# Kernel optimization log

Hardware: AMD Instinct MI355X
Metric: run time of the kernel (lower is better)

## Reference

```python
import jax, jax.numpy as jnp
import numpy as np

TAG_THR = 0.1
MIN_HEIGHT = 0.0
PULL_WEIGHT = 1.0
PUSH_WEIGHT = 1.0
EPS = 1e-6


def _bbox_iou(boxes):
    # boxes: [N,4] -> IoU [N,N] (standard, no +1 offset; heights in the loss
    # are also computed without +1)
    x1, y1, x2, y2 = boxes[:, 0], boxes[:, 1], boxes[:, 2], boxes[:, 3]
    area = (x2 - x1) * (y2 - y1)
    iw = jnp.clip(jnp.minimum(x2[:, None], x2[None, :]) - jnp.maximum(x1[:, None], x1[None, :]), 0.0)
    ih = jnp.clip(jnp.minimum(y2[:, None], y2[None, :]) - jnp.maximum(y1[:, None], y1[None, :]), 0.0)
    inter = iw * ih
    union = area[:, None] + area[None, :] - inter
    return inter / jnp.maximum(union, 1e-12)


def _single_image(pred, gt_inds, proposals):
    # pred [N,D], gt_inds [N] int, proposals [N,5]
    N = pred.shape[0]
    heights = proposals[:, 3] - proposals[:, 1]
    valid = (gt_inds >= 0) & (heights > MIN_HEIGHT)
    scores = proposals[:, 4]
    iou = _bbox_iou(proposals[:, :4])  # [N,N]

    def step(state, _):
        alive, tot_pull, tot_push, pull_cnt, push_cnt = state
        active = jnp.sum(alive) >= 2  # pop i; if nothing remains, the torch loop breaks
        # i = highest-scoring remaining proposal (greedy, score-sorted)
        i = jnp.argmax(jnp.where(alive, scores, -jnp.inf))
        rem = alive.at[i].set(False)
        overlap = (iou[i] > 0.0) & rem
        diff = jnp.mean((pred - pred[i]) ** 2, axis=1)  # [N]
        check = diff < TAG_THR
        same = gt_inds == gt_inds[i]
        pull_m = overlap & same & ~check
        push_m = overlap & ~same & check
        pn = jnp.sum(pull_m)
        qn = jnp.sum(push_m)
        pull_l = jnp.sum(jnp.where(pull_m, diff * scores, 0.0)) / jnp.maximum(pn, 1).astype(diff.dtype)
        push_l = jnp.sum(jnp.where(push_m, jnp.exp(-diff) * scores, 0.0)) / jnp.maximum(qn, 1).astype(diff.dtype)
        add_pull = active & (pn > 0)
        add_push = active & (qn > 0)
        tot_pull = tot_pull + jnp.where(add_pull, pull_l, 0.0)
        tot_push = tot_push + jnp.where(add_push, push_l, 0.0)
        pull_cnt = pull_cnt + add_pull.astype(jnp.float32)
        push_cnt = push_cnt + add_push.astype(jnp.float32)
        # suppress everything overlapping i whose tag is already close (diff < thr)
        new_alive = rem & ~(overlap & check)
        alive = jnp.where(active, new_alive, alive)
        return (alive, tot_pull, tot_push, pull_cnt, push_cnt), None

    z = jnp.float32(0.0)
    init = (valid, z, z, z, z)
    (_, tot_pull, tot_push, pull_cnt, push_cnt), _ = jax.lax.scan(step, init, None, length=N)
    pull = tot_pull / (pull_cnt + EPS)
    push = tot_push / (push_cnt + EPS)
    return push, pull


def setup_inputs() -> dict:
    key = jax.random.key(0)
    k1, k2, k3, k4, k5, k6, k7 = jax.random.split(key, 7)
    IMGS, N, D = 4, 2000, 4
    pred = jax.random.normal(k1, (IMGS, N, D), dtype=jnp.float32)
    gt_inds = jax.random.randint(k2, (IMGS, N), 0, 50, dtype=jnp.int32)
    x1 = jax.random.uniform(k3, (IMGS, N), minval=0.0, maxval=800.0)
    y1 = jax.random.uniform(k4, (IMGS, N), minval=0.0, maxval=800.0)
    w = jax.random.uniform(k5, (IMGS, N), minval=8.0, maxval=128.0)
    h = jax.random.uniform(k6, (IMGS, N), minval=8.0, maxval=128.0)
    score = jax.random.uniform(k7, (IMGS, N), minval=0.0, maxval=1.0)
    proposals = jnp.stack([x1, y1, x1 + w, y1 + h, score], axis=-1).astype(jnp.float32)
    gt_bboxes = jax.random.uniform(jax.random.fold_in(key, 9), (IMGS, 20, 4), dtype=jnp.float32)
    return {"pred": pred, "gt_inds": gt_inds, "proposals": proposals, "gt_bboxes": gt_bboxes}


def reference(pred, gt_inds, proposals, gt_bboxes):
    # gt_bboxes is accepted by the torch forward but never used in the loss math.
    push, pull = jax.vmap(_single_image)(pred, gt_inds, proposals)  # per-image scalars
    img_num = pred.shape[0]
    push_loss = jnp.sum(push) / img_num * PUSH_WEIGHT
    pull_loss = jnp.sum(pull) / img_num * PULL_WEIGHT
    return push_loss, pull_loss
```

## Files before the change

### kernel.cpp

```cpp
#include <hip/hip_runtime.h>
#include <stdint.h>

#define BLOCK 256
#define KMAX 8
#define NWAVES (BLOCK / 64)
#define S2 2048
#define NW 32
#define NCH 32
#define SPB 16
#define PB (S2 / SPB)
#define RB (S2 / BLOCK)
#define PCAP 65536
#define LDSP2 4096
#define BCAP 64
#define EFF_INF 0x7FFFFFFF

__global__ __launch_bounds__(BLOCK) void rankcount_kernel(
    const float* __restrict__ proposals,
    int* __restrict__ partial, int* __restrict__ pcnt,
    float* __restrict__ acc, int* __restrict__ done, int N, int imgs)
{
    const int bi = blockIdx.x, bj = blockIdx.y, img = blockIdx.z;
    const int t = threadIdx.x;
    if (bi == 0 && bj == 0 && img == 0) {
        if (t < imgs) pcnt[t] = 0;
        if (t >= 64 && t < 64 + imgs*4) acc[t - 64] = 0.f;
        if (t == 128) *done = 0;
    }
    const float* P = proposals + (size_t)img * N * 5;
    __shared__ unsigned sj[BLOCK];
    const int jbase = bj * BLOCK;
    {
        int j = jbase + t;
        sj[t] = (j < N) ? __float_as_uint(P[j*5 + 4]) : 0u;
    }
    __syncthreads();
    const int i = bi * BLOCK + t;
    if (i >= N) return;
    const unsigned my = __float_as_uint(P[i*5 + 4]);
    int p = 0;
    const uint4* s4 = (const uint4*)sj;
#pragma unroll
    for (int q = 0; q < BLOCK/4; ++q) {
        uint4 v = s4[q];
        int jj = jbase + q*4;
        p += (int)((v.x > my) | ((v.x == my) & (jj + 0 < i)));
        p += (int)((v.y > my) | ((v.y == my) & (jj + 1 < i)));
        p += (int)((v.z > my) | ((v.z == my) & (jj + 2 < i)));
        p += (int)((v.w > my) | ((v.w == my) & (jj + 3 < i)));
    }
    partial[((size_t)(img*RB + bj))*S2 + i] = p;
}

__global__ __launch_bounds__(BLOCK) void rankscatter_kernel(
    const float* __restrict__ pred, const int* __restrict__ gt_inds,
    const float* __restrict__ proposals, const int* __restrict__ partial,
    float* __restrict__ soa, int* __restrict__ sgt, int N, int imgs)
{
    const int img = blockIdx.y, t = threadIdx.x;
    const int i = blockIdx.x * BLOCK + t;
    const size_t stride = (size_t)imgs * S2;
    const size_t base   = (size_t)img * S2;

    if (i >= N) {
        if (i < S2) {
#pragma unroll
            for (int a = 0; a < 9; ++a) soa[(size_t)a*stride + base + i] = 0.f;
            sgt[base + i] = -1;
        }
        return;
    }

    const float* P = proposals + (size_t)img * N * 5;
    const float* E = pred      + (size_t)img * N * 4;
    const int*   G = gt_inds   + (size_t)img * N;

    const float p0 = P[i*5+0], p1 = P[i*5+1], p2 = P[i*5+2],
                p3 = P[i*5+3], p4 = P[i*5+4];
    const float q0 = E[i*4+0], q1 = E[i*4+1], q2 = E[i*4+2], q3 = E[i*4+3];
    const int   gg = G[i];

    int p = 0;
#pragma unroll
    for (int b = 0; b < RB; ++b)
        p += partial[((size_t)(img*RB + b))*S2 + i];

    soa[0*stride + base + p] = p0;
    soa[1*stride + base + p] = p1;
    soa[2*stride + base + p] = p2;
    soa[3*stride + base + p] = p3;
    soa[4*stride + base + p] = p4;
    soa[5*stride + base + p] = q0;
    soa[6*stride + base + p] = q1;
    soa[7*stride + base + p] = q2;
    soa[8*stride + base + p] = q3;
    sgt[base + p] = gg;
}

__global__ __launch_bounds__(BLOCK) void suppairs_kernel(
    const float* __restrict__ soa, unsigned* __restrict__ pairs,
    int* __restrict__ pcnt, int N, int imgs)
{
    const int ic = blockIdx.x, jc = blockIdx.y, img = blockIdx.z;
    if (ic < jc) return;
    const int t = threadIdx.x, wave = t >> 6, lane = t & 63;
    const size_t stride = (size_t)imgs * S2, base = (size_t)img * S2;
    __shared__ float si[8][64];
    for (int idx = t; idx < 512; idx += BLOCK) {
        int f = idx >> 6, e = idx & 63;
        int a = (f < 4) ? f : f + 1;
        si[f][e] = soa[(size_t)a*stride + base + ic*64 + e];
    }
    __syncthreads();
    const int j = jc*64 + lane;
    const float jx1 = soa[0*stride+base+j], jy1 = soa[1*stride+base+j];
    const float jx2 = soa[2*stride+base+j], jy2 = soa[3*stride+base+j];
    const float j0  = soa[5*stride+base+j], j1  = soa[6*stride+base+j];
    const float j2  = soa[7*stride+base+j], j3  = soa[8*stride+base+j];
    const bool jin = (j < N);
    unsigned* PL = pairs + (size_t)img * PCAP;
    for (int ii = 0; ii < 16; ++ii) {
        int il = wave*16 + ii;
        int i  = ic*64 + il;
        bool s = false;
        if (jin && i < N && i > j) {
            float iw = fminf(jx2, si[2][il]) - fmaxf(jx1, si[0][il]);
            float ih = fminf(jy2, si[3][il]) - fmaxf(jy1, si[1][il]);
            if (iw > 0.f && ih > 0.f) {
                float d0 = j0-si[4][il], d1 = j1-si[5][il];
                float d2 = j2-si[6][il], d3 = j3-si[7][il];
                float diff = 0.25f*(d0*d0 + d1*d1 + d2*d2 + d3*d3);
                s = diff < 0.1f;
            }
        }
        unsigned long long m = __ballot(s);
        if (m) {
            int leader = __ffsll((unsigned long long)m) - 1;
            int basei = 0;
            if (lane == leader) basei = atomicAdd(&pcnt[img], __popcll(m));
            basei = __shfl(basei, leader);
            if (s) {
                int idx = basei + __popcll(m & ((lane == 0) ? 0ull : (~0ull >> (64 - lane))));
                if (idx < PCAP) PL[idx] = ((unsigned)j << 11) | (unsigned)i;
            }
        }
    }
}

__global__ __launch_bounds__(BLOCK) void greedyeff_kernel(
    const unsigned* __restrict__ pairs, const int* __restrict__ pcnt,
    const int* __restrict__ sgt, const float* __restrict__ soa,
    unsigned long long* __restrict__ selw, int* __restrict__ eff,
    int* __restrict__ nsteps, int imgs)
{
    const int img = blockIdx.x, t = threadIdx.x;
    const int lane = t & 63, wave = t >> 6;
    const size_t stride = (size_t)imgs * S2, base = (size_t)img * S2;

    __shared__ __align__(16) char A[16384];
    __shared__ unsigned spair[LDSP2];
    __shared__ unsigned bucket[NCH * BCAP];
    __shared__ int bcnt[NCH];
    __shared__ unsigned long long skilled[NW], ssel[NW], svalid[NW];
    __shared__ int pfx[NW + 1];
    __shared__ unsigned wsum[NWAVES];
    __shared__ int bm[NWAVES];
    __shared__ int sV;

    unsigned long long* slocAll = (unsigned long long*)A;

    int P = pcnt[img]; if (P > PCAP) P = PCAP;
    const unsigned* PL = pairs + (size_t)img * PCAP;
    const bool staged = (P <= LDSP2);

    for (int x = t; x < S2; x += BLOCK) slocAll[x] = 0ull;
    if (t < NCH) bcnt[t] = 0;
    if (t == 0) sV = 0;
    __syncthreads();
    if (staged) for (int p = t; p < P; p += BLOCK) spair[p] = PL[p];
    for (int g = wave; g < NCH; g += NWAVES) {
        int j = g*64 + lane;
        int gv = sgt[base + j];
        float a = soa[1*stride + base + j];
        float b = soa[3*stride + base + j];
        bool invalid = !(gv >= 0 && (b - a) > 0.f);
        unsigned long long bb = __ballot(invalid);
        if (lane == 0) {
            skilled[g] = bb;
            svalid[g] = ~bb;
            atomicAdd(&sV, 64 - __popcll(bb));
        }
    }
    __syncthreads();
    for (int p = t; p < P; p += BLOCK) {
        unsigned v = staged ? spair[p] : PL[p];
        int lo = v >> 11, hi = v & 2047;
        if ((lo >> 6) == (hi >> 6)) {
            atomicOr(&slocAll[hi], 1ull << (lo & 63));
        } else {
            int idx = atomicAdd(&bcnt[lo >> 6], 1);
            if (idx < BCAP) bucket[(lo >> 6)*BCAP + idx] = v;
        }
    }
    __syncthreads();

    if (wave == 0) {
        const unsigned long long lowmask = (lane == 0) ? 0ull : (~0ull >> (64 - lane));
        for (int c = 0; c < NCH; ++c) {
            unsigned long long U = ~skilled[c];
            const unsigned long long loc = slocAll[c*64 + lane];
            unsigned long long sel = 0ull;
            while (U) {
                bool inU = (U >> lane) & 1ull;
                unsigned long long Am = __ballot(inU && ((loc & U & lowmask) == 0ull));
                sel |= Am;
                bool kill = inU && !((Am >> lane) & 1ull) && ((loc & Am) != 0ull);
                unsigned long long K = __ballot(kill);
                U &= ~(Am | K);
            }
            if (lane == 0) ssel[c] = sel;
            if (sel != 0ull) {
                const int bc = bcnt[c];
                if (bc <= BCAP) {
                    for (int q = lane; q < bc; q += 64) {
                        unsigned v = bucket[c*BCAP + q];
                        int lo = v >> 11, hi = v & 2047;
                        if ((sel >> (lo & 63)) & 1ull)
                            atomicOr(&skilled[hi >> 6], 1ull << (hi & 63));
                    }
                } else {
                    for (int p = lane; p < P; p += 64) {
                        unsigned v = PL[p];
                        int lo = v >> 11, hi = v & 2047;
                        if ((lo >> 6) == c && (hi >> 6) != c &&
                            ((sel >> (lo & 63)) & 1ull))
                            atomicOr(&skilled[hi >> 6], 1ull << (hi & 63));
                    }
                }
            }
        }
    }
    __syncthreads();
    if (t < NW) selw[(size_t)img*NW + t] = ssel[t];

    int* sistar = (int*)A;
    unsigned* hist = (unsigned*)(A + 8192);
    for (int x = t; x < S2; x += BLOCK) { sistar[x] = EFF_INF; hist[x] = 0u; }
    if (t == 0) {
        int s = 0;
        for (int w = 0; w < NW; ++w) { pfx[w] = s; s += __popcll(ssel[w]); }
        pfx[NW] = s;
    }
    __syncthreads();
    for (int p = t; p < P; p += BLOCK) {
        unsigned v = staged ? spair[p] : PL[p];
        int lo = v >> 11, hi = v & 2047;
        if ((ssel[lo >> 6] >> (lo & 63)) & 1ull) atomicMin(&sistar[hi], lo);
    }
    __syncthreads();
#pragma unroll
    for (int k = 0; k < 8; ++k) {
        const int j = k*BLOCK + t;
        const int jw = j >> 6, jb = j & 63;
        bool valid = (svalid[jw] >> jb) & 1ull;
        bool selb  = (ssel[jw] >> jb) & 1ull;
        int e;
        if (!valid) e = 0;
        else if (selb)
            e = pfx[jw] + __popcll(ssel[jw] & (jb ? (~0ull >> (64 - jb)) : 0ull));
        else {
            int is = sistar[j];
            if (is == EFF_INF) e = EFF_INF;
            else {
                int iw_ = is >> 6, ib = is & 63;
                e = pfx[iw_] + __popcll(ssel[iw_] & (ib ? (~0ull >> (64 - ib)) : 0ull)) + 1;
                atomicAdd(&hist[e - 1], 1u);
            }
        }
        eff[(size_t)img*S2 + j] = e;
    }
    __syncthreads();

    const int V = sV, Sc = pfx[NW];
    unsigned loc8[8]; unsigned s = 0;
#pragma unroll
    for (int k = 0; k < 8; ++k) { s += hist[t*8 + k]; loc8[k] = s; }
    unsigned tot = s;
    for (int o = 1; o < 64; o <<= 1) {
        unsigned u = __shfl_up(tot, o);
        if (lane >= o) tot += u;
    }
    if (lane == 63) wsum[wave] = tot;
    __syncthreads();
    unsigned woff = 0;
    for (int w = 0; w < wave; ++w) woff += wsum[w];
    unsigned exclP = woff + tot - s;
    __syncthreads();
#pragma unroll
    for (int k = 0; k < 8; ++k) hist[t*8 + k] = exclP + loc8[k];
    __syncthreads();
    int best = EFF_INF;
    for (int r = t; r < Sc; r += BLOCK) {
        unsigned rem = (r == 0) ? 0u : hist[r - 1];
        int alive = V - r - (int)rem;
        if (alive < 2) best = min(best, r);
    }
    for (int o = 32; o > 0; o >>= 1) best = min(best, __shfl_down(best, o));
    if (lane == 0) bm[wave] = best;
    __syncthreads();
    if (t == 0) {
        int b = bm[0];
        for (int w = 1; w < NWAVES; ++w) b = min(b, bm[w]);
        nsteps[img] = min(b, Sc);
    }
}

__global__ __launch_bounds__(BLOCK) void pairsfinal_kernel(
    const float* __restrict__ soa, const int* __restrict__ sgt,
    const int* __restrict__ eff, const unsigned long long* __restrict__ selw,
    const int* __restrict__ nsteps, float* __restrict__ acc,
    int* __restrict__ done, float* __restrict__ out, int imgs)
{
    const int ic = blockIdx.x, img = blockIdx.y;
    const int t = threadIdx.x, wave = t >> 6, lane = t & 63;
    const size_t stride = (size_t)imgs * S2, base = (size_t)img * S2;
    __shared__ unsigned long long ss[NW];
    __shared__ float pw[NWAVES][4];
    __shared__ int anyact, ticket;
    if (t < NW) ss[t] = selw[(size_t)img*NW + t];
    if (t == 0) anyact = 0;
    __syncthreads();
    const int ns = nsteps[img];

    float bx1[4], by1[4], bx2[4], by2[4], f0[4], f1[4], f2[4], f3[4];
    int bgt[4], rk[4]; bool act[4];
    bool any = false;
#pragma unroll
    for (int u = 0; u < 4; ++u) {
        const int i = ic*SPB + wave*4 + u;
        const int iw_ = i >> 6, ib = i & 63;
        bool selb = (ss[iw_] >> ib) & 1ull;
        int r = __popcll(ss[iw_] & (ib ? (~0ull >> (64 - ib)) : 0ull));
        for (int w = 0; w < iw_; ++w) r += __popcll(ss[w]);
        rk[u] = r;
        act[u] = selb && (r < ns);
        any |= act[u];
        if (act[u]) {
            bx1[u] = soa[0*stride+base+i]; by1[u] = soa[1*stride+base+i];
            bx2[u] = soa[2*stride+base+i]; by2[u] = soa[3*stride+base+i];
            f0[u]  = soa[5*stride+base+i]; f1[u]  = soa[6*stride+base+i];
            f2[u]  = soa[7*stride+base+i]; f3[u]  = soa[8*stride+base+i];
            bgt[u] = sgt[base + i];
        } else {
            bx1[u]=by1[u]=bx2[u]=by2[u]=0.f; f0[u]=f1[u]=f2[u]=f3[u]=0.f; bgt[u]=-2;
        }
    }
    if (any && lane == 0) anyact = 1;
    __syncthreads();

    if (anyact) {
        float ps[4] = {0,0,0,0}, pn[4] = {0,0,0,0};
        float qs[4] = {0,0,0,0}, qn[4] = {0,0,0,0};
        for (int jt = 0; jt < NCH; ++jt) {
            const int j = jt*64 + lane;
            const float jx1 = soa[0*stride+base+j], jy1 = soa[1*stride+base+j];
            const float jx2 = soa[2*stride+base+j], jy2 = soa[3*stride+base+j];
            const float jsc = soa[4*stride+base+j];
            const float j0  = soa[5*stride+base+j], j1  = soa[6*stride+base+j];
            const float j2  = soa[7*stride+base+j], j3  = soa[8*stride+base+j];
            const int   jgt = sgt[base + j];
            const int   jef = eff[(size_t)img*S2 + j];
#pragma unroll
            for (int u = 0; u < 4; ++u) {
                if (!act[u]) continue;
                if (rk[u] < jef) {
                    float iw = fminf(jx2, bx2[u]) - fmaxf(jx1, bx1[u]);
                    float ih = fminf(jy2, by2[u]) - fmaxf(jy1, by1[u]);
                    if (iw > 0.f && ih > 0.f) {
                        float d0 = j0 - f0[u], d1 = j1 - f1[u];
                        float d2 = j2 - f2[u], d3 = j3 - f3[u];
                        float diff = 0.25f*(d0*d0 + d1*d1 + d2*d2 + d3*d3);
                        bool check = diff < 0.1f;
                        bool same  = (jgt == bgt[u]);
                        if (same && !check)      { ps[u] += diff * jsc;       pn[u] += 1.f; }
                        else if (!same && check) { qs[u] += expf(-diff)*jsc;  qn[u] += 1.f; }
                    }
                }
            }
        }
        float sPull = 0.f, cPull = 0.f, sPush = 0.f, cPush = 0.f;
#pragma unroll
        for (int u = 0; u < 4; ++u) {
            if (!act[u]) continue;
            float a0 = ps[u], a1 = pn[u], a2 = qs[u], a3 = qn[u];
            for (int o = 32; o > 0; o >>= 1) {
                a0 += __shfl_down(a0, o); a1 += __shfl_down(a1, o);
                a2 += __shfl_down(a2, o); a3 += __shfl_down(a3, o);
            }
            if (lane == 0) {
                if (a1 > 0.f) { sPull += a0 / a1; cPull += 1.f; }
                if (a3 > 0.f) { sPush += a2 / a3; cPush += 1.f; }
            }
        }
        if (lane == 0) {
            pw[wave][0] = sPull; pw[wave][1] = cPull;
            pw[wave][2] = sPush; pw[wave][3] = cPush;
        }
        __syncthreads();
        if (t == 0) {
            float a = 0, b = 0, c = 0, d = 0;
            for (int w = 0; w < NWAVES; ++w) {
                a += pw[w][0]; b += pw[w][1]; c += pw[w][2]; d += pw[w][3];
            }
            if (a != 0.f) atomicAdd(&acc[img*4+0], a);
            if (b != 0.f) atomicAdd(&acc[img*4+1], b);
            if (c != 0.f) atomicAdd(&acc[img*4+2], c);
            if (d != 0.f) atomicAdd(&acc[img*4+3], d);
        }
    }

    __syncthreads();
    __threadfence();
    if (t == 0) ticket = atomicAdd(done, 1);
    __syncthreads();
    if (ticket == PB * imgs - 1 && t == 0) {
        __threadfence();
        float push = 0.f, pull = 0.f;
        for (int i = 0; i < imgs; ++i) {
            pull += acc[i*4+0] / (acc[i*4+1] + 1e-6f);
            push += acc[i*4+2] / (acc[i*4+3] + 1e-6f);
        }
        out[0] = push / (float)imgs;
        out[1] = pull / (float)imgs;
    }
}

__global__ __launch_bounds__(BLOCK) void tagloss_kernel(
    const float* __restrict__ pred, const int* __restrict__ gt_inds,
    const float* __restrict__ proposals, float* __restrict__ ws, int N)
{
    const int img = blockIdx.x, t = threadIdx.x;
    const int lane = t & 63, wav = t >> 6;
    const float* P = proposals + (size_t)img * N * 5;
    const float* E = pred      + (size_t)img * N * 4;
    const int*   G = gt_inds   + (size_t)img * N;
    float x1[KMAX], y1[KMAX], x2[KMAX], y2[KMAX], sc[KMAX];
    float e0[KMAX], e1[KMAX], e2[KMAX], e3[KMAX];
    int gt[KMAX]; unsigned amask = 0u; int local_alive = 0;
#pragma unroll
    for (int k = 0; k < KMAX; ++k) {
        int j = k * BLOCK + t;
        if (j < N) {
            x1[k]=P[j*5+0]; y1[k]=P[j*5+1]; x2[k]=P[j*5+2]; y2[k]=P[j*5+3]; sc[k]=P[j*5+4];
            e0[k]=E[j*4+0]; e1[k]=E[j*4+1]; e2[k]=E[j*4+2]; e3[k]=E[j*4+3]; gt[k]=G[j];
            if (gt[k] >= 0 && (y2[k]-y1[k]) > 0.0f) { amask |= 1u<<k; local_alive++; }
        } else { x1[k]=y1[k]=x2[k]=y2[k]=0.f; sc[k]=0.f; e0[k]=e1[k]=e2[k]=e3[k]=0.f; gt[k]=-1; }
    }
    __shared__ unsigned long long s_key[NWAVES];
    __shared__ float s_b[9];
    __shared__ float s_part[NWAVES][5];
    int alive_count;
    {
        float v = (float)local_alive;
#pragma unroll
        for (int o = 32; o > 0; o >>= 1) v += __shfl_down(v, o);
        if (lane == 0) s_part[wav][0] = v;
        __syncthreads();
        float tot = 0.f;
        for (int w = 0; w < NWAVES; ++w) tot += s_part[w][0];
        alive_count = (int)tot;
    }
    float tot_pull=0.f, tot_push=0.f, pull_cnt=0.f, push_cnt=0.f;
    while (alive_count >= 2) {
        unsigned long long key = 0ull;
#pragma unroll
        for (int k = 0; k < KMAX; ++k)
            if (amask & (1u<<k)) {
                unsigned long long kk = ((unsigned long long)__float_as_uint(sc[k])<<32)
                                      | (unsigned long long)(0xFFFFFFFFu - (unsigned)(k*BLOCK+t));
                if (kk > key) key = kk;
            }
#pragma unroll
        for (int o = 32; o > 0; o >>= 1) {
            unsigned long long ok = __shfl_down(key, o);
            if (ok > key) key = ok;
        }
        if (lane == 0) s_key[wav] = key;
        __syncthreads();
        unsigned long long bk = s_key[0];
        for (int w = 1; w < NWAVES; ++w) if (s_key[w] > bk) bk = s_key[w];
        const int i = (int)(0xFFFFFFFFu - (unsigned)(bk & 0xFFFFFFFFull));
        if ((i & (BLOCK-1)) == t) {
            int k = i / BLOCK;
            s_b[0]=x1[k]; s_b[1]=y1[k]; s_b[2]=x2[k]; s_b[3]=y2[k];
            s_b[4]=e0[k]; s_b[5]=e1[k]; s_b[6]=e2[k]; s_b[7]=e3[k];
            s_b[8]=__int_as_float(gt[k]);
        }
        __syncthreads();
        const float bx1=s_b[0], by1=s_b[1], bx2=s_b[2], by2=s_b[3];
        const float f0=s_b[4], f1=s_b[5], f2=s_b[6], f3=s_b[7];
        const int bgt = __float_as_int(s_b[8]);
        const float areai = (bx2-bx1)*(by2-by1);
        float psum=0.f,qsum=0.f,pn=0.f,qn=0.f,scnt=0.f;
#pragma unroll
        for (int k = 0; k < KMAX; ++k) {
            if (!(amask & (1u<<k))) continue;
            int j = k*BLOCK+t;
            if (j == i) { amask &= ~(1u<<k); continue; }
            float iw = fmaxf(fminf(x2[k],bx2)-fmaxf(x1[k],bx1),0.f);
            float ih = fmaxf(fminf(y2[k],by2)-fmaxf(y1[k],by1),0.f);
            float inter = iw*ih;
            float uni = (x2[k]-x1[k])*(y2[k]-y1[k]) + areai - inter;
            float iou = inter / fmaxf(uni, 1e-12f);
            if (iou > 0.f) {
                float d0=e0[k]-f0,d1=e1[k]-f1,d2=e2[k]-f2,d3=e3[k]-f3;
                float diff = 0.25f*(d0*d0+d1*d1+d2*d2+d3*d3);
                bool check = diff < 0.1f;
                bool same = (gt[k]==bgt);
                if (same && !check) { psum += diff*sc[k]; pn += 1.f; }
                if (!same && check) { qsum += __expf(-diff)*sc[k]; qn += 1.f; }
                if (check)          { amask &= ~(1u<<k); scnt += 1.f; }
            }
        }
        float r0=psum,r1=pn,r2=qsum,r3=qn,r4=scnt;
#pragma unroll
        for (int o = 32; o > 0; o >>= 1) {
            r0+=__shfl_down(r0,o); r1+=__shfl_down(r1,o); r2+=__shfl_down(r2,o);
            r3+=__shfl_down(r3,o); r4+=__shfl_down(r4,o);
        }
        if (lane == 0) { s_part[wav][0]=r0;s_part[wav][1]=r1;s_part[wav][2]=r2;s_part[wav][3]=r3;s_part[wav][4]=r4; }
        __syncthreads();
        float T0=0,T1=0,T2=0,T3=0,T4=0;
        for (int w = 0; w < NWAVES; ++w) {
            T0+=s_part[w][0];T1+=s_part[w][1];T2+=s_part[w][2];T3+=s_part[w][3];T4+=s_part[w][4];
        }
        if (T1 > 0.f) { tot_pull += T0/T1; pull_cnt += 1.f; }
        if (T3 > 0.f) { tot_push += T2/T3; push_cnt += 1.f; }
        alive_count -= 1 + (int)T4;
    }
    if (t == 0) {
        ws[img*2+0] = tot_push / (push_cnt + 1e-6f);
        ws[img*2+1] = tot_pull / (pull_cnt + 1e-6f);
    }
}

__global__ void finalize_fb_kernel(const float* __restrict__ ws,
                                   float* __restrict__ out, int imgs)
{
    if (threadIdx.x == 0 && blockIdx.x == 0) {
        float push = 0.f, pull = 0.f;
        for (int k = 0; k < imgs; ++k) { push += ws[2*k]; pull += ws[2*k+1]; }
        out[0] = push / (float)imgs;
        out[1] = pull / (float)imgs;
    }
}

extern "C" void kernel_launch(void* const* d_in, const int* in_sizes, int n_in,
                              void* d_out, int out_size, void* d_ws, size_t ws_size,
                              hipStream_t stream) {
    const float* pred      = (const float*)d_in[0];
    const int*   gt_inds   = (const int*)  d_in[1];
    const float* proposals = (const float*)d_in[2];
    const int imgs = in_sizes[3] / 80;
    const int N    = in_sizes[1] / imgs;

    size_t off = 0;
    auto alloc = [&](size_t b) { size_t o = off; off += (b + 255) & ~(size_t)255; return o; };
    const size_t soa_off  = alloc((size_t)9 * imgs * S2 * 4);
    const size_t sgt_off  = alloc((size_t)imgs * S2 * 4);
    const size_t sel_off  = alloc((size_t)imgs * NW * 8);
    const size_t eff_off  = alloc((size_t)imgs * S2 * 4);
    const size_t nst_off  = alloc((size_t)imgs * 4);
    const size_t rnk_off  = alloc((size_t)imgs * RB * S2 * 4);
    const size_t prs_off  = alloc((size_t)imgs * PCAP * 4);
    const size_t pcn_off  = alloc((size_t)imgs * 4);
    const size_t acc_off  = alloc((size_t)imgs * 16);
    const size_t don_off  = alloc(4);
    const size_t need = off;

    if (N <= S2 && imgs <= 8 && ws_size >= need) {
        char* w = (char*)d_ws;
        float*              soa  = (float*)(w + soa_off);
        int*                sgt  = (int*)(w + sgt_off);
        unsigned long long* sel  = (unsigned long long*)(w + sel_off);
        int*                eff  = (int*)(w + eff_off);
        int*                nst  = (int*)(w + nst_off);
        int*                rnk  = (int*)(w + rnk_off);
        unsigned*           prs  = (unsigned*)(w + prs_off);
        int*                pcn  = (int*)(w + pcn_off);
        float*              acc  = (float*)(w + acc_off);
        int*                don  = (int*)(w + don_off);

        rankcount_kernel<<<dim3(RB, RB, imgs), BLOCK, 0, stream>>>(
            proposals, rnk, pcn, acc, don, N, imgs);
        rankscatter_kernel<<<dim3(RB, imgs), BLOCK, 0, stream>>>(
            pred, gt_inds, proposals, rnk, soa, sgt, N, imgs);
        suppairs_kernel<<<dim3(NCH, NCH, imgs), BLOCK, 0, stream>>>(
            soa, prs, pcn, N, imgs);
        greedyeff_kernel<<<imgs, BLOCK, 0, stream>>>(prs, pcn, sgt, soa,
                                                     sel, eff, nst, imgs);
        pairsfinal_kernel<<<dim3(PB, imgs), BLOCK, 0, stream>>>(
            soa, sgt, eff, sel, nst, acc, don, (float*)d_out, imgs);
    } else {
        float* ws = (float*)d_ws;
        tagloss_kernel<<<imgs, BLOCK, 0, stream>>>(pred, gt_inds, proposals, ws, N);
        finalize_fb_kernel<<<1, 64, 0, stream>>>(ws, (float*)d_out, imgs);
    }
}
```

Before: 152.5 us.

## Split pair-loss j-range across blocks with per-selection accumulators and final ratio kernel

The pairs kernel now splits the candidate j-range into four slices across an extra grid dimension. Partial pull and push sums and counts are accumulated atomically into a per-selected-proposal buffer, which rankcount zeroes. A new single-block kernel then computes the per-proposal ratios and the final losses. This replaces the ticket-based last-block reduction and takes the rank directly from eff instead of recomputing popcounts. The aim is more parallelism for the long j loop, at the cost of an extra launch, more global atomics and a larger zeroed workspace.

```diff
diff --git a/kernel.cpp b/kernel.cpp
--- a/kernel.cpp
+++ b/kernel.cpp
@@ -9,6 +9,8 @@
 #define NCH 32
 #define SPB 16
 #define PB (S2 / SPB)
+#define JS 4
+#define JCH (NCH / JS)
 #define RB (S2 / BLOCK)
 #define PCAP 65536
 #define LDSP2 4096
@@ -18,14 +20,16 @@
 __global__ __launch_bounds__(BLOCK) void rankcount_kernel(
     const float* __restrict__ proposals,
     int* __restrict__ partial, int* __restrict__ pcnt,
-    float* __restrict__ acc, int* __restrict__ done, int N, int imgs)
+    float* __restrict__ selacc, int N, int imgs)
 {
     const int bi = blockIdx.x, bj = blockIdx.y, img = blockIdx.z;
     const int t = threadIdx.x;
-    if (bi == 0 && bj == 0 && img == 0) {
-        if (t < imgs) pcnt[t] = 0;
-        if (t >= 64 && t < 64 + imgs*4) acc[t - 64] = 0.f;
-        if (t == 128) *done = 0;
+    if (bi == 0 && bj == 0 && img == 0 && t < imgs) pcnt[t] = 0;
+    if (bj == 0) {
+        const int id = img * RB + bi;
+#pragma unroll
+        for (int k = 0; k < 4; ++k)
+            selacc[(size_t)id * 1024 + k * 256 + t] = 0.f;
     }
     const float* P = proposals + (size_t)img * N * 5;
     __shared__ unsigned sj[BLOCK];
@@ -315,18 +319,16 @@
     }
 }
 
-__global__ __launch_bounds__(BLOCK) void pairsfinal_kernel(
+__global__ __launch_bounds__(BLOCK) void pairsacc_kernel(
     const float* __restrict__ soa, const int* __restrict__ sgt,
     const int* __restrict__ eff, const unsigned long long* __restrict__ selw,
-    const int* __restrict__ nsteps, float* __restrict__ acc,
-    int* __restrict__ done, float* __restrict__ out, int imgs)
-{
-    const int ic = blockIdx.x, img = blockIdx.y;
+    const int* __restrict__ nsteps, float* __restrict__ selacc, int imgs)
+{
+    const int ic = blockIdx.x, js = blockIdx.y, img = blockIdx.z;
     const int t = threadIdx.x, wave = t >> 6, lane = t & 63;
     const size_t stride = (size_t)imgs * S2, base = (size_t)img * S2;
     __shared__ unsigned long long ss[NW];
-    __shared__ float pw[NWAVES][4];
-    __shared__ int anyact, ticket;
+    __shared__ int anyact;
     if (t < NW) ss[t] = selw[(size_t)img*NW + t];
     if (t == 0) anyact = 0;
     __syncthreads();
@@ -338,12 +340,10 @@
 #pragma unroll
     for (int u = 0; u < 4; ++u) {
         const int i = ic*SPB + wave*4 + u;
-        const int iw_ = i >> 6, ib = i & 63;
-        bool selb = (ss[iw_] >> ib) & 1ull;
-        int r = __popcll(ss[iw_] & (ib ? (~0ull >> (64 - ib)) : 0ull));
-        for (int w = 0; w < iw_; ++w) r += __popcll(ss[w]);
-        rk[u] = r;
-        act[u] = selb && (r < ns);
+        bool selb = (ss[i >> 6] >> (i & 63)) & 1ull;
+        int e = eff[(size_t)img*S2 + i];
+        rk[u] = e;
+        act[u] = selb && (e < ns);
         any |= act[u];
         if (act[u]) {
             bx1[u] = soa[0*stride+base+i]; by1[u] = soa[1*stride+base+i];
@@ -357,78 +357,75 @@
     }
     if (any && lane == 0) anyact = 1;
     __syncthreads();
-
-    if (anyact) {
-        float ps[4] = {0,0,0,0}, pn[4] = {0,0,0,0};
-        float qs[4] = {0,0,0,0}, qn[4] = {0,0,0,0};
-        for (int jt = 0; jt < NCH; ++jt) {
-            const int j = jt*64 + lane;
-            const float jx1 = soa[0*stride+base+j], jy1 = soa[1*stride+base+j];
-            const float jx2 = soa[2*stride+base+j], jy2 = soa[3*stride+base+j];
-            const float jsc = soa[4*stride+base+j];
-            const float j0  = soa[5*stride+base+j], j1  = soa[6*stride+base+j];
-            const float j2  = soa[7*stride+base+j], j3  = soa[8*stride+base+j];
-            const int   jgt = sgt[base + j];
-            const int   jef = eff[(size_t)img*S2 + j];
-#pragma unroll
-            for (int u = 0; u < 4; ++u) {
-                if (!act[u]) continue;
-                if (rk[u] < jef) {
-                    float iw = fminf(jx2, bx2[u]) - fmaxf(jx1, bx1[u]);
-                    float ih = fminf(jy2, by2[u]) - fmaxf(jy1, by1[u]);
-                    if (iw > 0.f && ih > 0.f) {
-                        float d0 = j0 - f0[u], d1 = j1 - f1[u];
-                        float d2 = j2 - f2[u], d3 = j3 - f3[u];
-                        float diff = 0.25f*(d0*d0 + d1*d1 + d2*d2 + d3*d3);
-                        bool check = diff < 0.1f;
-                        bool same  = (jgt == bgt[u]);
-                        if (same && !check)      { ps[u] += diff * jsc;       pn[u] += 1.f; }
-                        else if (!same && check) { qs[u] += expf(-diff)*jsc;  qn[u] += 1.f; }
-                    }
-                }
-            }
-        }
-        float sPull = 0.f, cPull = 0.f, sPush = 0.f, cPush = 0.f;
+    if (!anyact) return;
+
+    float ps[4] = {0,0,0,0}, pn[4] = {0,0,0,0};
+    float qs[4] = {0,0,0,0}, qn[4] = {0,0,0,0};
+    for (int jt = 0; jt < JCH; ++jt) {
+        const int j = (js*JCH + jt)*64 + lane;
+        const float jx1 = soa[0*stride+base+j], jy1 = soa[1*stride+base+j];
+        const float jx2 = soa[2*stride+base+j], jy2 = soa[3*stride+base+j];
+        const float jsc = soa[4*stride+base+j];
+        const float j0  = soa[5*stride+base+j], j1  = soa[6*stride+base+j];
+        const float j2  = soa[7*stride+base+j], j3  = soa[8*stride+base+j];
+        const int   jgt = sgt[base + j];
+        const int   jef = eff[(size_t)img*S2 + j];
 #pragma unroll
         for (int u = 0; u < 4; ++u) {
             if (!act[u]) continue;
-            float a0 = ps[u], a1 = pn[u], a2 = qs[u], a3 = qn[u];
-            for (int o = 32; o > 0; o >>= 1) {
-                a0 += __shfl_down(a0, o); a1 += __shfl_down(a1, o);
-                a2 += __shfl_down(a2, o); a3 += __shfl_down(a3, o);
-            }
-            if (lane == 0) {
-                if (a1 > 0.f) { sPull += a0 / a1; cPull += 1.f; }
-                if (a3 > 0.f) { sPush += a2 / a3; cPush += 1.f; }
-            }
+            if (rk[u] < jef) {
+                float iw = fminf(jx2, bx2[u]) - fmaxf(jx1, bx1[u]);
+                float ih = fminf(jy2, by2[u]) - fmaxf(jy1, by1[u]);
+                if (iw > 0.f && ih > 0.f) {
+                    float d0 = j0 - f0[u], d1 = j1 - f1[u];
+                    float d2 = j2 - f2[u], d3 = j3 - f3[u];
+                    float diff = 0.25f*(d0*d0 + d1*d1 + d2*d2 + d3*d3);
+                    bool check = diff < 0.1f;
+                    bool same  = (jgt == bgt[u]);
+                    if (same && !check)      { ps[u] += diff * jsc;       pn[u] += 1.f; }
+                    else if (!same && check) { qs[u] += expf(-diff)*jsc;  qn[u] += 1.f; }
+                }
+            }
+        }
+    }
+#pragma unroll
+    for (int u = 0; u < 4; ++u) {
+        if (!act[u]) continue;
+        float a0 = ps[u], a1 = pn[u], a2 = qs[u], a3 = qn[u];
+        for (int o = 32; o > 0; o >>= 1) {
+            a0 += __shfl_down(a0, o); a1 += __shfl_down(a1, o);
+            a2 += __shfl_down(a2, o); a3 += __shfl_down(a3, o);
         }
         if (lane == 0) {
-            pw[wave][0] = sPull; pw[wave][1] = cPull;
-            pw[wave][2] = sPush; pw[wave][3] = cPush;
-        }
-        __syncthreads();
-        if (t == 0) {
-            float a = 0, b = 0, c = 0, d = 0;
-            for (int w = 0; w < NWAVES; ++w) {
-                a += pw[w][0]; b += pw[w][1]; c += pw[w][2]; d += pw[w][3];
-            }
-            if (a != 0.f) atomicAdd(&acc[img*4+0], a);
-            if (b != 0.f) atomicAdd(&acc[img*4+1], b);
-            if (c != 0.f) atomicAdd(&acc[img*4+2], c);
-            if (d != 0.f) atomicAdd(&acc[img*4+3], d);
-        }
-    }
-
-    __syncthreads();
-    __threadfence();
-    if (t == 0) ticket = atomicAdd(done, 1);
-    __syncthreads();
-    if (ticket == PB * imgs - 1 && t == 0) {
-        __threadfence();
+            const int i = ic*SPB + wave*4 + u;
+            float* p = selacc + ((size_t)img*S2 + i) * 4;
+            if (a1 != 0.f) atomicAdd(&p[0], a0);
+            if (a1 != 0.f) atomicAdd(&p[1], a1);
+            if (a3 != 0.f) atomicAdd(&p[2], a2);
+            if (a3 != 0.f) atomicAdd(&p[3], a3);
+        }
+    }
+}
+
+__global__ __launch_bounds__(BLOCK) void ratiofinal_kernel(
+    const float* __restrict__ selacc, float* __restrict__ out, int imgs)
+{
+    const int t = threadIdx.x;
+    __shared__ float a[8][4];
+    if (t < 32) ((float*)a)[t] = 0.f;
+    __syncthreads();
+    for (int e = t; e < imgs * S2; e += BLOCK) {
+        const float4 v = ((const float4*)selacc)[e];
+        const int img = e >> 11;
+        if (v.y > 0.f) { atomicAdd(&a[img][0], v.x / v.y); atomicAdd(&a[img][1], 1.f); }
+        if (v.w > 0.f) { atomicAdd(&a[img][2], v.z / v.w); atomicAdd(&a[img][3], 1.f); }
+    }
+    __syncthreads();
+    if (t == 0) {
         float push = 0.f, pull = 0.f;
         for (int i = 0; i < imgs; ++i) {
-            pull += acc[i*4+0] / (acc[i*4+1] + 1e-6f);
-            push += acc[i*4+2] / (acc[i*4+3] + 1e-6f);
+            pull += a[i][0] / (a[i][1] + 1e-6f);
+            push += a[i][2] / (a[i][3] + 1e-6f);
         }
         out[0] = push / (float)imgs;
         out[1] = pull / (float)imgs;
@@ -574,8 +571,7 @@
     const size_t rnk_off  = alloc((size_t)imgs * RB * S2 * 4);
     const size_t prs_off  = alloc((size_t)imgs * PCAP * 4);
     const size_t pcn_off  = alloc((size_t)imgs * 4);
-    const size_t acc_off  = alloc((size_t)imgs * 16);
-    const size_t don_off  = alloc(4);
+    const size_t sac_off  = alloc((size_t)imgs * S2 * 16);
     const size_t need = off;
 
     if (N <= S2 && imgs <= 8 && ws_size >= need) {
@@ -588,19 +584,19 @@
         int*                rnk  = (int*)(w + rnk_off);
         unsigned*           prs  = (unsigned*)(w + prs_off);
         int*                pcn  = (int*)(w + pcn_off);
-        float*              acc  = (float*)(w + acc_off);
-        int*                don  = (int*)(w + don_off);
+        float*              sac  = (float*)(w + sac_off);
 
         rankcount_kernel<<<dim3(RB, RB, imgs), BLOCK, 0, stream>>>(
-            proposals, rnk, pcn, acc, don, N, imgs);
+            proposals, rnk, pcn, sac, N, imgs);
         rankscatter_kernel<<<dim3(RB, imgs), BLOCK, 0, stream>>>(
             pred, gt_inds, proposals, rnk, soa, sgt, N, imgs);
         suppairs_kernel<<<dim3(NCH, NCH, imgs), BLOCK, 0, stream>>>(
             soa, prs, pcn, N, imgs);
         greedyeff_kernel<<<imgs, BLOCK, 0, stream>>>(prs, pcn, sgt, soa,
                                                      sel, eff, nst, imgs);
-        pairsfinal_kernel<<<dim3(PB, imgs), BLOCK, 0, stream>>>(
-            soa, sgt, eff, sel, nst, acc, don, (float*)d_out, imgs);
+        pairsacc_kernel<<<dim3(PB, JS, imgs), BLOCK, 0, stream>>>(
+            soa, sgt, eff, sel, nst, sac, imgs);
+        ratiofinal_kernel<<<1, BLOCK, 0, stream>>>(sac, (float*)d_out, imgs);
     } else {
         float* ws = (float*)d_ws;
         tagloss_kernel<<<imgs, BLOCK, 0, stream>>>(pred, gt_inds, proposals, ws, N);
```

Measured after the change: 141.1 us. 7.5% less time.
